# Kernel optimization log

Hardware: AMD Instinct MI355X
Metric: run time of the kernel (lower is better)

The kernel has to match this reference:

```python
import jax, jax.numpy as jnp
import numpy as np

N, D, V = 4096, 256, 32000
B, T = 32, 256
U_DECAY, X_DECAY = 0.97, 0.97
EPS = 1e-6


def layernorm_row(z):
    # matches torch: (z - mean) / (std + eps), std with Bessel correction (ddof=1)
    m = jnp.mean(z, axis=-1, keepdims=True)
    s = jnp.std(z, axis=-1, keepdims=True, ddof=1)
    return (z - m) / (s + EPS)


def setup_inputs() -> dict:
    key = jax.random.key(0)
    k1, k2, k3, k4, k5 = jax.random.split(key, 5)
    token_emb = jax.random.normal(k1, (V, D), jnp.float32) / np.float32(np.sqrt(D))
    E = jax.random.normal(k2, (D, N), jnp.float32) / np.float32(np.sqrt(N))
    Dx = jax.random.normal(k3, (N, D), jnp.float32) / np.float32(np.sqrt(D))
    Dy = jax.random.normal(k4, (N, D), jnp.float32) / np.float32(np.sqrt(D))
    idx = jax.random.randint(k5, (B, T), 0, V)
    return {"idx": idx, "token_emb": token_emb, "E": E, "Dx": Dx, "Dy": Dy}


def reference(idx, token_emb, E, Dx, Dy):
    b = idx.shape[0]

    def step(carry, tok):
        x, rho = carry                                   # x: (b,n), rho: (b,d,n)
        v_prev = token_emb[tok]                          # (b,d) embedding gather
        x_t = X_DECAY * x + jax.nn.relu(v_prev @ Dx.T)   # (b,n)
        x_t = x_t / (jnp.sum(jnp.abs(x_t), axis=-1, keepdims=True) + EPS)  # L1 normalize
        a_star = jnp.einsum('bdn,bn->bd', rho, x_t)      # fast-weight readout
        y_t = jax.nn.relu(layernorm_row(a_star) @ Dy.T) * jax.nn.relu(x_t)  # (b,n)
        v_star = layernorm_row(y_t @ E.T)                # (b,d)
        # Hebbian decayed outer-product memory update
        rho = U_DECAY * (rho + jnp.einsum('bd,bn->bdn', layernorm_row(v_prev), x_t))
        return (x_t, rho), v_star

    x0 = jnp.zeros((b, N), jnp.float32)
    rho0 = jnp.zeros((b, D, N), jnp.float32)
    (_, _), vs = jax.lax.scan(step, (x0, rho0), idx.T)   # vs: (T,b,d)
    return jnp.transpose(vs, (1, 0, 2))                  # (b,T,d)
```

## Files before the change

### kernel.cpp

```cpp
#include <hip/hip_runtime.h>
#include <hip/hip_bf16.h>

#define NN 4096
#define DD 256
#define BB 32
#define TT 256
#define EPS 1e-6f
#define DECAY 0.97f
#define LOG2_DECAY -0.043943348f

typedef __hip_bfloat16 bf16;
typedef short short8 __attribute__((ext_vector_type(8)));
typedef float floatx4 __attribute__((ext_vector_type(4)));

__device__ __forceinline__ float bfu2f(short u) {
    return __uint_as_float(((unsigned)(unsigned short)u) << 16);
}

__device__ __forceinline__ float blk_sum_256(float v, volatile float* s4) {
#pragma unroll
    for (int o = 32; o > 0; o >>= 1) v += __shfl_down(v, o, 64);
    int lane = threadIdx.x & 63, w = threadIdx.x >> 6;
    __syncthreads();
    if (lane == 0) s4[w] = v;
    __syncthreads();
    return s4[0] + s4[1] + s4[2] + s4[3];
}

__device__ __forceinline__ void gl16(const bf16* g, bf16* l) {
    __builtin_amdgcn_global_load_lds((const __attribute__((address_space(1))) void*)g,
                                     (__attribute__((address_space(3))) void*)l, 16, 0, 0);
}

__global__ void k_detect(const unsigned short* __restrict__ raw, int* __restrict__ flag) {
    __shared__ int cnt[4];
    int tid = threadIdx.x;
    int bad = 0;
    for (int i = tid; i < 8192; i += 256) {
        unsigned int u = raw[2 * i];
        float v = __uint_as_float(u << 16);
        if (!(fabsf(v) < 1e6f)) bad++;
    }
#pragma unroll
    for (int o = 32; o > 0; o >>= 1) bad += __shfl_down(bad, o, 64);
    int lane = tid & 63, w = tid >> 6;
    if (lane == 0) cnt[w] = bad;
    __syncthreads();
    if (tid == 0) flag[0] = (cnt[0] + cnt[1] + cnt[2] + cnt[3] < 32) ? 1 : 0;
}

__global__ __launch_bounds__(256) void k_convert3(const void* __restrict__ s0,
                                                  const void* __restrict__ s1,
                                                  const void* __restrict__ s2,
                                                  bf16* __restrict__ d0,
                                                  bf16* __restrict__ d1,
                                                  bf16* __restrict__ d2,
                                                  const int* __restrict__ flag) {
    const int per = NN * DD / 8;
    int i = blockIdx.x * 256 + threadIdx.x;
    int m = i / per, j = i % per;
    const void* s = (m == 0) ? s0 : (m == 1) ? s1 : s2;
    bf16* d = (m == 0) ? d0 : (m == 1) ? d1 : d2;
    if (flag[0]) {
        ((uint4*)d)[j] = ((const uint4*)s)[j];
    } else {
        const float4* f = (const float4*)s;
        float4 a = f[2 * j], b = f[2 * j + 1];
        short8 o;
        float va[8] = {a.x, a.y, a.z, a.w, b.x, b.y, b.z, b.w};
#pragma unroll
        for (int k = 0; k < 8; k++) {
            bf16 t = __float2bfloat16(va[k]);
            o[k] = *reinterpret_cast<short*>(&t);
        }
        ((short8*)d)[j] = o;
    }
}

__global__ __launch_bounds__(256) void k_gather_ln(const void* __restrict__ emb,
                                                   const int* __restrict__ idx,
                                                   bf16* __restrict__ Vpb,
                                                   bf16* __restrict__ Ub,
                                                   const int* __restrict__ flag) {
    __shared__ float s4[4];
    int r = blockIdx.x, d = threadIdx.x;
    int tok = idx[r];
    long o = (long)tok * DD + d;
    float e = flag[0] ? __bfloat162float(((const bf16*)emb)[o]) : ((const float*)emb)[o];
    Vpb[(long)r * DD + d] = __float2bfloat16(e);
    float m = blk_sum_256(e, s4) * (1.0f / DD);
    float zc = e - m;
    float var = blk_sum_256(zc * zc, s4) * (1.0f / (DD - 1));
    Ub[(long)r * DD + d] = __float2bfloat16(zc / (sqrtf(fmaxf(var, 0.f)) + EPS));
}

__global__ __launch_bounds__(256) void k_transpose(const bf16* __restrict__ Ub,
                                                   bf16* __restrict__ Ut) {
    __shared__ bf16 tile[32][33];
    int b = blockIdx.z;
    int t0 = blockIdx.x * 32, d0 = blockIdx.y * 32;
    const bf16* src = Ub + (long)b * TT * DD;
    bf16* dst = Ut + (long)b * DD * TT;
    int rr = threadIdx.x >> 3, c4 = (threadIdx.x & 7) * 4;
#pragma unroll
    for (int i = 0; i < 4; i++) tile[rr][c4 + i] = src[(long)(t0 + rr) * DD + d0 + c4 + i];
    __syncthreads();
#pragma unroll
    for (int i = 0; i < 4; i++) dst[(long)(d0 + rr) * TT + t0 + c4 + i] = tile[c4 + i][rr];
}

enum { EPI_RELU_BF16 = 0, EPI_NONE_F32 = 1, EPI_RELU_MULX_BF16 = 2 };

template <int EPI, int KSPLIT, int TRI, int SWZ>
__global__ __launch_bounds__(256) void k_mfma_nt(int K,
                                                 const bf16* __restrict__ A, int lda, long sA,
                                                 const bf16* __restrict__ B, int ldb, long sB,
                                                 void* __restrict__ Cv, int ldc, long sC,
                                                 const bf16* __restrict__ Xaux,
                                                 float* __restrict__ Wsum) {
    __shared__ __align__(16) char smem[49152];
    bf16* R = (bf16*)smem;

    int z = blockIdx.z;
    int bz = z / KSPLIT, ks = z % KSPLIT;
    A += (long)bz * sA;
    B += (long)bz * sB;
    int bx = blockIdx.x, by = blockIdx.y;
    if (TRI) {
        by = (blockIdx.x >= 1) ? 1 : 0;
        bx = (blockIdx.x == 2) ? 1 : 0;
    }
    if (SWZ) {
        int gx = gridDim.x;
        int nwg = gx * gridDim.y;
        int id = by * gx + bx;
        int q = nwg >> 3;
        int nid = (id & 7) * q + (id >> 3);
        bx = nid % gx;
        by = nid / gx;
    }
    int bm = by * 128, bn = bx * 128;
    int tid = threadIdx.x;
    int srow = tid >> 2;
    int scol = ((((srow >> 1) & 3) ^ (tid & 3)) << 3);
    int w = tid >> 6, lane = tid & 63;
    int wm = (w >> 1) * 64, wn = (w & 1) * 64;
    int lm = lane & 15, kh = lane >> 4;

    floatx4 acc[4][4];
#pragma unroll
    for (int i = 0; i < 4; i++)
#pragma unroll
        for (int j = 0; j < 4; j++) acc[i][j] = (floatx4){0.f, 0.f, 0.f, 0.f};

    int kchunk = K / KSPLIT;
    int kbeg = ks * kchunk, kend = kbeg + kchunk;
    const bf16* gA0 = A + (long)(bm + srow) * lda + scol;
    const bf16* gA1 = gA0 + (long)64 * lda;
    const bf16* gB0 = B + (long)(bn + srow) * ldb + scol;
    const bf16* gB1 = gB0 + (long)64 * ldb;
    int dslot = tid * 8;

#define STAGE_SLOT(SBASE, KK)                          \
    {                                                  \
        bf16* bufA = (bf16*)(SBASE);                   \
        bf16* bufB = bufA + 4096;                      \
        gl16(gA0 + (KK), bufA + dslot);                \
        gl16(gA1 + (KK), bufA + 2048 + dslot);         \
        gl16(gB0 + (KK), bufB + dslot);                \
        gl16(gB1 + (KK), bufB + 2048 + dslot);         \
    }

    STAGE_SLOT(smem, kbeg);
    if (kbeg + 32 < kend) STAGE_SLOT(smem + 16384, kbeg + 32);

    int cur = 0;
    for (int k0 = kbeg; k0 < kend; k0 += 32) {
        __builtin_amdgcn_s_barrier();
        __builtin_amdgcn_sched_barrier(0);
        if (k0 + 64 < kend) {
            int ps = (cur == 0) ? 2 : cur - 1;
            STAGE_SLOT(smem + ps * 16384, k0 + 64);
        }
        int rem = (kend - k0 - 32) >> 5;
        if (rem >= 2)      asm volatile("s_waitcnt vmcnt(8)" ::: "memory");
        else if (rem == 1) asm volatile("s_waitcnt vmcnt(4)" ::: "memory");
        else               asm volatile("s_waitcnt vmcnt(0)" ::: "memory");
        __builtin_amdgcn_s_barrier();
        __builtin_amdgcn_sched_barrier(0);
        bf16* cbA = (bf16*)(smem + cur * 16384);
        bf16* cbB = cbA + 4096;
        short8 af[4], bfr[4];
#pragma unroll
        for (int i = 0; i < 4; i++) {
            int row = wm + i * 16 + lm;
            af[i] = *(const short8*)(cbA + row * 32 + ((((row >> 1) & 3) ^ kh) << 3));
        }
#pragma unroll
        for (int j = 0; j < 4; j++) {
            int row = wn + j * 16 + lm;
            bfr[j] = *(const short8*)(cbB + row * 32 + ((((row >> 1) & 3) ^ kh) << 3));
        }
#pragma unroll
        for (int i = 0; i < 4; i++)
#pragma unroll
            for (int j = 0; j < 4; j++)
                acc[i][j] = __builtin_amdgcn_mfma_f32_16x16x32_bf16(af[i], bfr[j], acc[i][j], 0, 0, 0);
        cur = (cur == 2) ? 0 : cur + 1;
    }
#undef STAGE_SLOT

    if (EPI == EPI_NONE_F32) {
        long cbase = (long)z * sC;
#pragma unroll
        for (int i = 0; i < 4; i++)
#pragma unroll
            for (int j = 0; j < 4; j++)
#pragma unroll
                for (int r = 0; r < 4; r++) {
                    int gm = bm + wm + i * 16 + kh * 4 + r;
                    int gn = bn + wn + j * 16 + lm;
                    ((float*)Cv)[cbase + (long)gm * ldc + gn] = acc[i][j][r];
                }
        return;
    }

#pragma unroll
    for (int p = 0; p < 2; p++) {
        __syncthreads();
        if ((w >> 1) == p) {
#pragma unroll
            for (int i = 0; i < 4; i++)
#pragma unroll
                for (int j = 0; j < 4; j++)
#pragma unroll
                    for (int r = 0; r < 4; r++) {
                        int rr = i * 16 + kh * 4 + r;
                        int cc = wn + j * 16 + lm;
                        R[rr * 136 + cc] = __float2bfloat16(fmaxf(acc[i][j][r], 0.f));
                    }
        }
        __syncthreads();
#pragma unroll
        for (int it = 0; it < 4; it++) {
            int row_l = it * 16 + (tid >> 4);
            int c8 = (tid & 15) * 8;
            short8 vv = *(const short8*)(R + row_l * 136 + c8);
            int gm = bm + p * 64 + row_l;
            long off = (long)gm * ldc + bn + c8;
            if (EPI == EPI_RELU_BF16) {
                *(short8*)((bf16*)Cv + off) = vv;
                float s = 0.f;
#pragma unroll
                for (int k = 0; k < 8; k++) s += bfu2f(vv[k]);
#pragma unroll
                for (int o = 8; o > 0; o >>= 1) s += __shfl_down(s, o, 16);
                if ((tid & 15) == 0) atomicAdd(&Wsum[gm], s);
            } else {
                short8 xx = *(const short8*)(Xaux + off);
                short8 oo;
#pragma unroll
                for (int k = 0; k < 8; k++) {
                    float prod = bfu2f(vv[k]) * fmaxf(bfu2f(xx[k]), 0.f);
                    bf16 t = __float2bfloat16(prod);
                    oo[k] = *reinterpret_cast<short*>(&t);
                }
                *(short8*)((bf16*)Cv + off) = oo;
            }
        }
    }
}

__global__ __launch_bounds__(256) void k_scalar_scan(const float* __restrict__ Wsum,
                                                     float* __restrict__ invS) {
    __shared__ float sw[BB * TT];
    for (int i = threadIdx.x; i < BB * TT; i += 256) sw[i] = Wsum[i];
    __syncthreads();
    int b = threadIdx.x;
    if (b < BB) {
        float sig = 0.f;
        for (int t = 0; t < TT; t++) {
            float S = DECAY * sig + sw[b * TT + t];
            float inv = 1.f / (S + EPS);
            invS[b * TT + t] = inv;
            sig = S * inv;
        }
    }
}

__global__ __launch_bounds__(256) void k_colscan(bf16* __restrict__ W,
                                                 const float* __restrict__ invS) {
    __shared__ float sv[TT];
    int b = blockIdx.y;
    sv[threadIdx.x] = invS[b * TT + threadIdx.x];
    __syncthreads();
    int n = blockIdx.x * 256 + threadIdx.x;
    bf16* p = W + (long)b * TT * NN + n;
    float x = 0.f;
    for (int t = 0; t < TT; t++) {
        float w = __bfloat162float(p[(long)t * NN]);
        x = (DECAY * x + w) * sv[t];
        p[(long)t * NN] = __float2bfloat16(x);
    }
}

__global__ __launch_bounds__(256) void k_reduce_mask(const float* __restrict__ Gp,
                                                     bf16* __restrict__ G) {
    int r = blockIdx.x;
    int b = r >> 8, t = r & 255;
    int s = threadIdx.x;
    long base = ((long)b * 4) * 65536 + (long)t * 256 + s;
    float v = Gp[base] + Gp[base + 65536] + Gp[base + 2 * 65536] + Gp[base + 3 * 65536];
    float o = (s < t) ? v * exp2f((float)(t - s) * LOG2_DECAY) : 0.f;
    G[(long)r * 256 + s] = __float2bfloat16(o);
}

__global__ __launch_bounds__(256) void k_ln_rows(const float* __restrict__ Zp,
                                                 bf16* __restrict__ O) {
    __shared__ float s4[4];
    long r = blockIdx.x;
    int d = threadIdx.x;
    long b = r >> 8, t = r & 255;
    long base = (b * 2) * 65536 + t * 256 + d;
    float z = Zp[base] + Zp[base + 65536];
    float m = blk_sum_256(z, s4) * (1.0f / DD);
    float zc = z - m;
    float var = blk_sum_256(zc * zc, s4) * (1.0f / (DD - 1));
    O[r * DD + d] = __float2bfloat16(zc / (sqrtf(fmaxf(var, 0.f)) + EPS));
}

__global__ __launch_bounds__(256) void k_final_ln(const float* __restrict__ Zp,
                                                  void* __restrict__ out,
                                                  const int* __restrict__ flag) {
    __shared__ float s4[4];
    long r = blockIdx.x;
    int d = threadIdx.x;
    const long SL = (long)8192 * 256;
    long o = r * DD + d;
    float z = Zp[o] + Zp[o + SL] + Zp[o + 2 * SL] + Zp[o + 3 * SL];
    float m = blk_sum_256(z, s4) * (1.0f / DD);
    float zc = z - m;
    float var = blk_sum_256(zc * zc, s4) * (1.0f / (DD - 1));
    float v = zc / (sqrtf(fmaxf(var, 0.f)) + EPS);
    if (flag[0]) ((bf16*)out)[o] = __float2bfloat16(v);
    else ((float*)out)[o] = v;
}

extern "C" void kernel_launch(void* const* d_in, const int* in_sizes, int n_in,
                              void* d_out, int out_size, void* d_ws, size_t ws_size,
                              hipStream_t stream) {
    const int* idx = (const int*)d_in[0];
    const void* emb = d_in[1];
    const void* E = d_in[2];
    const void* Dx = d_in[3];
    const void* Dy = d_in[4];

    char* base = (char*)d_ws;
    size_t off = 0;
    int* flag = (int*)base; off += 1024;
    bf16* Dxb = (bf16*)(base + off); off += (size_t)NN * DD * 2;
    bf16* Dyb = (bf16*)(base + off); off += (size_t)NN * DD * 2;
    bf16* Eb  = (bf16*)(base + off); off += (size_t)DD * NN * 2;
    bf16* Vpb = (bf16*)(base + off); off += (size_t)BB * TT * DD * 2;
    bf16* Ub  = (bf16*)(base + off); off += (size_t)BB * TT * DD * 2;
    bf16* Ut  = (bf16*)(base + off); off += (size_t)BB * TT * DD * 2;
    float* Wsum = (float*)(base + off); off += (size_t)BB * TT * 4;
    float* invS = (float*)(base + off); off += (size_t)BB * TT * 4;
    bf16* ALNb = (bf16*)(base + off); off += (size_t)BB * TT * DD * 2;
    bf16* G = (bf16*)(base + off); off += (size_t)BB * TT * TT * 2;
    float* Gp = (float*)(base + off); off += (size_t)4 * BB * TT * TT * 4;
    float* Astar = Gp;
    float* Zp = Gp;
    bf16* Xb = (bf16*)(base + off); off += (size_t)BB * TT * NN * 2;

    const int M = BB * TT;

    k_detect<<<1, 256, 0, stream>>>((const unsigned short*)emb, flag);
    k_convert3<<<3 * NN * DD / 8 / 256, 256, 0, stream>>>(Dx, Dy, E, Dxb, Dyb, Eb, flag);
    k_gather_ln<<<M, 256, 0, stream>>>(emb, idx, Vpb, Ub, flag);
    k_transpose<<<dim3(8, 8, BB), 256, 0, stream>>>(Ub, Ut);

    hipMemsetAsync(Wsum, 0, (size_t)M * 4, stream);

    k_mfma_nt<EPI_RELU_BF16, 1, 0, 1><<<dim3(32, 64, 1), 256, 0, stream>>>(
        DD, Vpb, DD, 0, Dxb, DD, 0, Xb, NN, 0, nullptr, Wsum);

    k_scalar_scan<<<1, 256, 0, stream>>>(Wsum, invS);
    k_colscan<<<dim3(16, BB, 1), 256, 0, stream>>>(Xb, invS);

    k_mfma_nt<EPI_NONE_F32, 4, 1, 0><<<dim3(3, 1, BB * 4), 256, 0, stream>>>(
        NN, Xb, NN, (long)TT * NN, Xb, NN, (long)TT * NN, Gp, TT, (long)TT * TT, nullptr, nullptr);
    k_reduce_mask<<<M, 256, 0, stream>>>(Gp, G);

    k_mfma_nt<EPI_NONE_F32, 2, 0, 0><<<dim3(2, 2, BB * 2), 256, 0, stream>>>(
        TT, G, TT, (long)TT * TT, Ut, TT, (long)DD * TT, Astar, DD, (long)TT * DD, nullptr, nullptr);
    k_ln_rows<<<M, 256, 0, stream>>>(Astar, ALNb);

    k_mfma_nt<EPI_RELU_MULX_BF16, 1, 0, 1><<<dim3(32, 64, 1), 256, 0, stream>>>(
        DD, ALNb, DD, 0, Dyb, DD, 0, Xb, NN, 0, Xb, nullptr);

    k_mfma_nt<EPI_NONE_F32, 4, 0, 1><<<dim3(2, 64, 4), 256, 0, stream>>>(
        NN, Xb, NN, 0, Eb, NN, 0, Zp, DD, (long)M * DD, nullptr, nullptr);

    k_final_ln<<<M, 256, 0, stream>>>(Zp, d_out, flag);
}
```

Measured before the change: 310.2 us.

## Add specialized full-K GEMM kernel for K=256 projections with register-prefetched B

Adds a dedicated kernel for the two M=8192, N=4096, K=256 GEMMs. It loads the whole 128x256 A tile into swizzled LDS with one async copy, then streams B fragments straight from global memory into registers with double buffering. This avoids the generic kernel's per-k-step LDS staging and barriers. It uses 64KB of LDS per block, which can reduce occupancy, and direct global loads of B may expose latency.

```diff
diff --git a/kernel.cpp b/kernel.cpp
--- a/kernel.cpp
+++ b/kernel.cpp
@@ -111,6 +111,136 @@
 
 enum { EPI_RELU_BF16 = 0, EPI_NONE_F32 = 1, EPI_RELU_MULX_BF16 = 2 };
 
+template <int EPI>
+__global__ __launch_bounds__(256) void k_fullk(const bf16* __restrict__ A,
+                                               const bf16* __restrict__ B,
+                                               bf16* __restrict__ C,
+                                               const bf16* __restrict__ Xaux,
+                                               float* __restrict__ Wsum) {
+    __shared__ __align__(16) char smem[65536];
+    bf16* As = (bf16*)smem;
+    bf16* R = (bf16*)smem;
+
+    int bx = blockIdx.x, by = blockIdx.y;
+    {
+        int gx = gridDim.x;
+        int nwg = gx * gridDim.y;
+        int id = by * gx + bx;
+        int q = nwg >> 3;
+        int nid = (id & 7) * q + (id >> 3);
+        bx = nid % gx;
+        by = nid / gx;
+    }
+    int bm = by * 128, bn = bx * 128;
+    int tid = threadIdx.x, w = tid >> 6, lane = tid & 63;
+    int wm = (w >> 1) * 64, wn = (w & 1) * 64;
+    int lm = lane & 15, kh = lane >> 4;
+
+    {
+        const bf16* Ab = A + (long)bm * DD;
+#pragma unroll
+        for (int g = 0; g < 16; g++) {
+            int idx = g * 256 + tid;
+            int row = idx >> 5, s = idx & 31;
+            gl16(Ab + (long)row * DD + ((s ^ (row & 7)) << 3), As + idx * 8);
+        }
+    }
+
+    const bf16* Bw = B + (long)(bn + wn + lm) * DD + kh * 8;
+    short8 b0[4], b1[4];
+#pragma unroll
+    for (int j = 0; j < 4; j++) b0[j] = *(const short8*)(Bw + (long)j * 16 * DD + 0 * 32);
+#pragma unroll
+    for (int j = 0; j < 4; j++) b1[j] = *(const short8*)(Bw + (long)j * 16 * DD + 1 * 32);
+
+    floatx4 acc[4][4];
+#pragma unroll
+    for (int i = 0; i < 4; i++)
+#pragma unroll
+        for (int j = 0; j < 4; j++) acc[i][j] = (floatx4){0.f, 0.f, 0.f, 0.f};
+
+    __syncthreads();
+
+#pragma unroll
+    for (int k = 0; k < 8; k++) {
+        short8 af[4];
+#pragma unroll
+        for (int i = 0; i < 4; i++) {
+            int r = wm + i * 16 + lm;
+            int slot = (4 * k + kh) ^ (r & 7);
+            af[i] = *(const short8*)(As + r * 256 + slot * 8);
+        }
+        if ((k & 1) == 0) {
+#pragma unroll
+            for (int i = 0; i < 4; i++)
+#pragma unroll
+                for (int j = 0; j < 4; j++)
+                    acc[i][j] = __builtin_amdgcn_mfma_f32_16x16x32_bf16(af[i], b0[j], acc[i][j], 0, 0, 0);
+            if (k < 6) {
+#pragma unroll
+                for (int j = 0; j < 4; j++)
+                    b0[j] = *(const short8*)(Bw + (long)j * 16 * DD + (k + 2) * 32);
+            }
+        } else {
+#pragma unroll
+            for (int i = 0; i < 4; i++)
+#pragma unroll
+                for (int j = 0; j < 4; j++)
+                    acc[i][j] = __builtin_amdgcn_mfma_f32_16x16x32_bf16(af[i], b1[j], acc[i][j], 0, 0, 0);
+            if (k < 6) {
+#pragma unroll
+                for (int j = 0; j < 4; j++)
+                    b1[j] = *(const short8*)(Bw + (long)j * 16 * DD + (k + 2) * 32);
+            }
+        }
+    }
+
+#pragma unroll
+    for (int p = 0; p < 2; p++) {
+        __syncthreads();
+        if ((w >> 1) == p) {
+#pragma unroll
+            for (int i = 0; i < 4; i++)
+#pragma unroll
+                for (int j = 0; j < 4; j++)
+#pragma unroll
+                    for (int r = 0; r < 4; r++) {
+                        int rr = i * 16 + kh * 4 + r;
+                        int cc = wn + j * 16 + lm;
+                        R[rr * 136 + cc] = __float2bfloat16(fmaxf(acc[i][j][r], 0.f));
+                    }
+        }
+        __syncthreads();
+#pragma unroll
+        for (int it = 0; it < 4; it++) {
+            int row_l = it * 16 + (tid >> 4);
+            int c8 = (tid & 15) * 8;
+            short8 vv = *(const short8*)(R + row_l * 136 + c8);
+            int gm = bm + p * 64 + row_l;
+            long off = (long)gm * NN + bn + c8;
+            if (EPI == EPI_RELU_BF16) {
+                *(short8*)(C + off) = vv;
+                float s = 0.f;
+#pragma unroll
+                for (int k = 0; k < 8; k++) s += bfu2f(vv[k]);
+#pragma unroll
+                for (int o = 8; o > 0; o >>= 1) s += __shfl_down(s, o, 16);
+                if ((tid & 15) == 0) atomicAdd(&Wsum[gm], s);
+            } else {
+                short8 xx = *(const short8*)(Xaux + off);
+                short8 oo;
+#pragma unroll
+                for (int k = 0; k < 8; k++) {
+                    float prod = bfu2f(vv[k]) * fmaxf(bfu2f(xx[k]), 0.f);
+                    bf16 t = __float2bfloat16(prod);
+                    oo[k] = *reinterpret_cast<short*>(&t);
+                }
+                *(short8*)(C + off) = oo;
+            }
+        }
+    }
+}
+
 template <int EPI, int KSPLIT, int TRI, int SWZ>
 __global__ __launch_bounds__(256) void k_mfma_nt(int K,
                                                  const bf16* __restrict__ A, int lda, long sA,
@@ -382,8 +512,7 @@
 
     hipMemsetAsync(Wsum, 0, (size_t)M * 4, stream);
 
-    k_mfma_nt<EPI_RELU_BF16, 1, 0, 1><<<dim3(32, 64, 1), 256, 0, stream>>>(
-        DD, Vpb, DD, 0, Dxb, DD, 0, Xb, NN, 0, nullptr, Wsum);
+    k_fullk<EPI_RELU_BF16><<<dim3(32, 64), 256, 0, stream>>>(Vpb, Dxb, Xb, nullptr, Wsum);
 
     k_scalar_scan<<<1, 256, 0, stream>>>(Wsum, invS);
     k_colscan<<<dim3(16, BB, 1), 256, 0, stream>>>(Xb, invS);
@@ -396,8 +525,7 @@
         TT, G, TT, (long)TT * TT, Ut, TT, (long)DD * TT, Astar, DD, (long)TT * DD, nullptr, nullptr);
     k_ln_rows<<<M, 256, 0, stream>>>(Astar, ALNb);
 
-    k_mfma_nt<EPI_RELU_MULX_BF16, 1, 0, 1><<<dim3(32, 64, 1), 256, 0, stream>>>(
-        DD, ALNb, DD, 0, Dyb, DD, 0, Xb, NN, 0, Xb, nullptr);
+    k_fullk<EPI_RELU_MULX_BF16><<<dim3(32, 64), 256, 0, stream>>>(ALNb, Dyb, Xb, Xb, nullptr);
 
     k_mfma_nt<EPI_NONE_F32, 4, 0, 1><<<dim3(2, 64, 4), 256, 0, stream>>>(
         NN, Xb, NN, 0, Eb, NN, 0, Zp, DD, (long)M * DD, nullptr, nullptr);
```

After: 336.4 us. +8.4%, slower.
